# Kernel optimization log

Measured on AMD Instinct MI355X. Metric: run time of the kernel, lower is better.

Reference implementation:

```python
import jax, jax.numpy as jnp
import numpy as np
from jax import lax

MIN_R = 0.01
RADIUS = 0.8
NSAMPLE = 32
PRED_NSAMPLE = 16
TEMPERATURE = 1.0
DIV_COEF = 10.0
GRID3 = 64  # grid_size**3, grid_size=4
EPS = 1e-5


def _ball_query(q, xyz, radius, nsample):
    """q (M,3), xyz (N,3), radius scalar or (M,). Returns idx (M,nsample) int32, empty (M,) bool.
    Mirrors stack ball_query CUDA op: first-found neighbors within radius, padded with first index."""
    N = xyz.shape[0]
    d2 = jnp.sum((q[:, None, :] - xyz[None, :, :]) ** 2, axis=-1)  # (M,N)
    r = jnp.broadcast_to(jnp.asarray(radius, d2.dtype), (q.shape[0],))[:, None]
    valid = d2 < r * r
    score = jnp.where(valid, -jnp.arange(N, dtype=jnp.int32), -(N + 1))
    vals, _ = lax.top_k(score, nsample)  # largest score == smallest valid index
    idx = -vals
    pad = idx == (N + 1)
    idx = jnp.where(pad, idx[:, :1], idx)  # pad with first found neighbor
    empty = pad[:, 0]                       # no neighbor at all
    idx = jnp.where(empty[:, None], 0, idx)
    return idx, empty


def _group(q, xyz, feats, idx, empty):
    """QueryAndGroup gather: relative xyz concat point features; zero empty queries.
    Returns (M, nsample, 3+C)."""
    g_xyz = xyz[idx] - q[:, None, :]
    g = jnp.concatenate([g_xyz, feats[idx]], axis=-1)
    return jnp.where(empty[:, None, None], jnp.zeros((), g.dtype), g)


def _mlp(x, params):
    """Shared 1x1 Conv2d + BatchNorm2d(training stats) + ReLU stack. x: (B,M,S,C)."""
    for W, g, b in params:
        x = jnp.einsum('bmsc,cd->bmsd', x, W)
        mu = x.mean(axis=(0, 1, 2))
        var = x.var(axis=(0, 1, 2))
        x = (x - mu) * lax.rsqrt(var + EPS) * g + b
        x = jax.nn.relu(x)
    return x


def setup_inputs() -> dict:
    key = jax.random.key(0)
    ks = jax.random.split(key, 16)
    B, N, C, R, Croi = 2, 8192, 32, 64, 128
    scene = jnp.array([10.0, 10.0, 4.0], jnp.float32)
    xyz = jax.random.uniform(ks[0], (B, N, 3), jnp.float32) * scene
    features = jax.random.normal(ks[1], (B, N, C), jnp.float32)
    rois = jax.random.uniform(ks[2], (B, R, GRID3, 3), jnp.float32) * scene
    roi_features = jax.random.normal(ks[3], (B, R, Croi), jnp.float32)

    def kaiming(k, fi, fo):
        return jax.random.normal(k, (fi, fo), jnp.float32) * np.float32(np.sqrt(2.0 / fi))

    return {
        'xyz': xyz, 'features': features, 'rois': rois, 'roi_features': roi_features,
        'temperature_decay': jnp.ones((1,), jnp.float32),
        # predict mlp: [32+3, 32, 32]
        'pw0': kaiming(ks[4], 35, 32), 'pg0': jnp.ones(32), 'pb0': jnp.zeros(32),
        'pw1': kaiming(ks[5], 32, 32), 'pg1': jnp.ones(32), 'pb1': jnp.zeros(32),
        # feat mlp: [32+3, 64, 64]
        'fw0': kaiming(ks[6], 35, 64), 'fg0': jnp.ones(64), 'fb0': jnp.zeros(64),
        'fw1': kaiming(ks[7], 64, 64), 'fg1': jnp.ones(64), 'fb1': jnp.zeros(64),
        # predict fc: [32*64 + 128, 1]
        'fcw': kaiming(ks[8], 2176, 1), 'fcb': jnp.zeros(1),
    }


def reference(xyz, features, rois, roi_features, temperature_decay,
              pw0, pg0, pb0, pw1, pg1, pb1,
              fw0, fg0, fb0, fw1, fg1, fb1, fcw, fcb):
    B, num_rois = rois.shape[0], rois.shape[1]
    new_xyz = rois.reshape(B, -1, 3)  # (B, M, 3), M = num_rois*grid^3

    # ---- radius-prediction branch: fixed-radius grouping + MLP + max-pool ----
    idx_p, empty_p = jax.vmap(lambda q, x: _ball_query(q, x, RADIUS, PRED_NSAMPLE))(new_xyz, xyz)
    gp = jax.vmap(_group)(new_xyz, xyz, features, idx_p, empty_p)  # (B,M,S,3+C)
    gp = _mlp(gp, [(pw0, pg0, pb0), (pw1, pg1, pb1)])
    pooled = gp.max(axis=2)                       # (B, M, Cp)
    pooled = pooled.reshape(B, num_rois, -1)      # (B, R, grid^3*Cp)
    res = jnp.concatenate([pooled, roi_features], axis=-1) @ fcw + fcb  # (B,R,1)
    r = jnp.maximum(res / DIV_COEF + RADIUS, MIN_R)
    r_pts = jnp.broadcast_to(r, (B, num_rois, GRID3)).reshape(B, -1)    # (B, M)

    # ---- deformable branch: per-query radius grouping + soft weights ----
    idx_d, empty_d = jax.vmap(lambda q, x, rr: _ball_query(q, x, rr, NSAMPLE))(new_xyz, xyz, r_pts)
    gd = jax.vmap(_group)(new_xyz, xyz, features, idx_d, empty_d)       # (B,M,S,3+C)
    dist = jnp.linalg.norm(gd[..., :3], axis=-1)                        # (B,M,S)
    w = jax.nn.sigmoid((r_pts[..., None] - dist) / (TEMPERATURE * temperature_decay[0]))
    w = jnp.where(empty_d[..., None], jnp.zeros((), w.dtype), w)
    gd = _mlp(gd, [(fw0, fg0, fb0), (fw1, fg1, fb1)])                   # (B,M,S,Cout)
    new_feats = (w[..., None] * gd).max(axis=2)                          # (B,M,Cout)

    return new_xyz.reshape(-1, 3), new_feats.reshape(-1, new_feats.shape[-1])
```

## Files before the change

kernel.cpp:

```cpp
#include <hip/hip_runtime.h>
#include <hip/hip_fp16.h>

#define NB 2
#define NPTS 8192
#define NQ 4096
#define MTOT 8192
#define SP 16
#define SD 32
#define CIN 32
#define CP 32
#define CF 64
#define NROI 128
#define RADIUS_C 0.8f
#define MIN_R_C 0.01f
#define DIV_COEF_C 10.0f

#define INV_CS 1.25f
#define NCX 13
#define NCY 13
#define NCZ 5
#define NCELL (NCX * NCY * NCZ)

__device__ int    g_idx_p[MTOT * SP];
__device__ int    g_empty_p[MTOT];
__device__ int    g_idx_d[MTOT * SD];
__device__ int    g_empty_d[MTOT];
__device__ int    g_cellcnt[NB][NCELL];
__device__ int    g_cellcur[NB][NCELL];
__device__ int    g_cellstart[NB][NCELL + 1];
__device__ float4 g_cellxyzw[NB][NPTS];
__device__ unsigned char g_xa[(size_t)MTOT * SD * CF * 2];
__device__ unsigned char g_xb[(size_t)MTOT * SD * CF * 2];
__device__ unsigned int g_w1h[CF * CF / 2];
__device__ float g_psT[CF * 2048];
__device__ float g_pqT[CF * 2048];
__device__ float g_bnscale[4][CF];
__device__ float g_bnshift[4][CF];
__device__ float g_pdot[MTOT];
__device__ float g_rroi[NROI];

typedef _Float16 h2v __attribute__((ext_vector_type(2)));
__device__ __forceinline__ float fdot2f(unsigned int a, unsigned int b, float c) {
#if defined(__has_builtin)
#if __has_builtin(__builtin_amdgcn_fdot2)
    h2v ha, hb;
    ha = *(h2v*)&a; hb = *(h2v*)&b;
    return __builtin_amdgcn_fdot2(ha, hb, c, false);
#else
    __half2 ha = *(__half2*)&a, hb = *(__half2*)&b;
    float2 fa = __half22float2(ha), fb = __half22float2(hb);
    return fmaf(fa.x, fb.x, fmaf(fa.y, fb.y, c));
#endif
#else
    __half2 ha = *(__half2*)&a, hb = *(__half2*)&b;
    float2 fa = __half22float2(ha), fb = __half22float2(hb);
    return fmaf(fa.x, fb.x, fmaf(fa.y, fb.y, c));
#endif
}

__global__ void copy_xyz_kernel(const float* __restrict__ rois, float* __restrict__ out) {
    int i = blockIdx.x * 256 + threadIdx.x;
    if (i < MTOT * 3) out[i] = rois[i];
}

__global__ void prep_w1_kernel(const float* __restrict__ fw1) {
    int i = blockIdx.x * 256 + threadIdx.x;
    if (i >= CF * CF / 2) return;
    int ch = i >> 5, c2 = i & 31;
    __half2 h = __floats2half2_rn(fw1[(2 * c2) * CF + ch], fw1[(2 * c2 + 1) * CF + ch]);
    g_w1h[i] = *(unsigned int*)&h;
}

__global__ void grid_zero_kernel() {
    int i = blockIdx.x * 1024 + threadIdx.x;
    if (i < NB * NCELL) ((int*)g_cellcnt)[i] = 0;
}

__device__ __forceinline__ int cell_of(float x, float y, float z) {
    int cx = min(NCX - 1, max(0, (int)floorf(x * INV_CS)));
    int cy = min(NCY - 1, max(0, (int)floorf(y * INV_CS)));
    int cz = min(NCZ - 1, max(0, (int)floorf(z * INV_CS)));
    return (cz * NCY + cy) * NCX + cx;
}

__global__ void grid_count_kernel(const float* __restrict__ xyz) {
    int i = blockIdx.x * 256 + threadIdx.x;
    int b = i >> 13;
    int cell = cell_of(xyz[(size_t)i * 3 + 0], xyz[(size_t)i * 3 + 1], xyz[(size_t)i * 3 + 2]);
    atomicAdd(&g_cellcnt[b][cell], 1);
}

__global__ void grid_prefix_kernel() {
    __shared__ int sc[1024];
    int b = blockIdx.x, tid = threadIdx.x;
    int v = (tid < NCELL) ? g_cellcnt[b][tid] : 0;
    sc[tid] = v;
    __syncthreads();
    for (int off = 1; off < 1024; off <<= 1) {
        int add = (tid >= off) ? sc[tid - off] : 0;
        __syncthreads();
        sc[tid] += add;
        __syncthreads();
    }
    if (tid < NCELL) {
        int excl = sc[tid] - v;
        g_cellstart[b][tid] = excl;
        g_cellcur[b][tid] = excl;
    }
    if (tid == 0) g_cellstart[b][NCELL] = NPTS;
}

__global__ void grid_scatter_kernel(const float* __restrict__ xyz) {
    int i = blockIdx.x * 256 + threadIdx.x;
    int b = i >> 13, il = i & (NPTS - 1);
    float x = xyz[(size_t)i * 3 + 0];
    float y = xyz[(size_t)i * 3 + 1];
    float z = xyz[(size_t)i * 3 + 2];
    int cell = cell_of(x, y, z);
    int pos = atomicAdd(&g_cellcur[b][cell], 1);
    g_cellxyzw[b][pos] = make_float4(x, y, z, __int_as_float(il));
}

template <int NS>
__launch_bounds__(256, 8)
__global__ void bq_grid_kernel(const float* __restrict__ xyz, const float* __restrict__ newxyz) {
    __shared__ int s_epos[4][1024];
    int tid = threadIdx.x, wv = tid >> 6, lane = tid & 63;
    int q = blockIdx.x * 4 + wv;
    int b = q >> 12;
    float qx = newxyz[q * 3 + 0], qy = newxyz[q * 3 + 1], qz = newxyz[q * 3 + 2];
    float r = (NS == SP) ? RADIUS_C : g_rroi[q >> 6];
    float r2 = r * r;
    int* idx_out   = (NS == SP) ? g_idx_p   : g_idx_d;
    int* empty_out = (NS == SP) ? g_empty_p : g_empty_d;

    float rp = r + 1e-4f;
    int xlo = max(0, min(NCX - 1, (int)floorf((qx - rp) * INV_CS)));
    int xhi = max(0, min(NCX - 1, (int)floorf((qx + rp) * INV_CS)));
    int ylo = max(0, min(NCY - 1, (int)floorf((qy - rp) * INV_CS)));
    int yhi = max(0, min(NCY - 1, (int)floorf((qy + rp) * INV_CS)));
    int zlo = max(0, min(NCZ - 1, (int)floorf((qz - rp) * INV_CS)));
    int zhi = max(0, min(NCZ - 1, (int)floorf((qz + rp) * INV_CS)));
    int nx = xhi - xlo + 1, ny = yhi - ylo + 1, nz = zhi - zlo + 1;
    int ncell = nx * ny * nz;

    int T = 0;
    bool fb = (ncell > 512);
    if (!fb) {
        for (int c0 = 0; c0 < ncell; c0 += 64) {
            int ci = c0 + lane;
            int cstart = 0, ccnt = 0;
            if (ci < ncell) {
                int cx = xlo + (ci % nx);
                int t1 = ci / nx;
                int cy = ylo + (t1 % ny);
                int cz = zlo + (t1 / ny);
                int cell = (cz * NCY + cy) * NCX + cx;
                cstart = g_cellstart[b][cell];
                ccnt = g_cellstart[b][cell + 1] - cstart;
            }
            int incl = ccnt;
#pragma unroll
            for (int off = 1; off < 64; off <<= 1) {
                int n = __shfl_up(incl, off, 64);
                if (lane >= off) incl += n;
            }
            int chunkT = __shfl(incl, 63, 64);
            int pre = T + incl - ccnt;
            if (T + chunkT <= 1024) {
                for (int k = 0; k < ccnt; ++k) s_epos[wv][pre + k] = cstart + k;
            }
            T += chunkT;
        }
        if (T > 1024) fb = true;
    }

    if (fb) {
        const float* xb = xyz + (size_t)b * NPTS * 3;
        int cnt2 = 0, first_idx = 0;
        for (int g = 0; g < NPTS / 64 && cnt2 < NS; ++g) {
            int p = (g << 6) + lane;
            float dx = qx - xb[3 * p + 0];
            float dy = qy - xb[3 * p + 1];
            float dz = qz - xb[3 * p + 2];
            bool valid = (dx * dx + dy * dy + dz * dz) < r2;
            unsigned long long mask = __ballot(valid);
            if (cnt2 == 0 && mask) first_idx = (g << 6) + (int)__builtin_ctzll(mask);
            int pos = cnt2 + __popcll(mask & ((1ull << lane) - 1ull));
            if (valid && pos < NS) idx_out[q * NS + pos] = p;
            cnt2 += (int)__popcll(mask);
        }
        if (cnt2 == 0) {
            if (lane < NS) idx_out[q * NS + lane] = 0;
            if (lane == 0) empty_out[q] = 1;
        } else {
            int filled = cnt2 < NS ? cnt2 : NS;
            if (lane >= filled && lane < NS) idx_out[q * NS + lane] = first_idx;
            if (lane == 0) empty_out[q] = 0;
        }
        return;
    }
    __asm__ volatile("s_waitcnt lgkmcnt(0)" ::: "memory");

    int p[16];
#pragma unroll
    for (int k = 0; k < 16; ++k) {
        int t = k * 64 + lane;
        int pk = 0x7FFFFFFF;
        if (t < T) {
            int e = s_epos[wv][t];
            float4 v = g_cellxyzw[b][e];
            float dx = qx - v.x, dy = qy - v.y, dz = qz - v.z;
            if (dx * dx + dy * dy + dz * dz < r2) pk = __float_as_int(v.w);
        }
        p[k] = pk;
    }

    int lcnt = 0, lmin = 0x7FFFFFFF;
#pragma unroll
    for (int k = 0; k < 16; ++k) {
        if (p[k] != 0x7FFFFFFF) { ++lcnt; lmin = min(lmin, p[k]); }
    }
    int cnt = lcnt, fidx = lmin;
#pragma unroll
    for (int off = 1; off < 64; off <<= 1) {
        cnt += __shfl_xor(cnt, off, 64);
        fidx = min(fidx, __shfl_xor(fidx, off, 64));
    }
    if (cnt == 0) {
        if (lane < NS) idx_out[q * NS + lane] = 0;
        if (lane == 0) empty_out[q] = 1;
        return;
    }
    int thr = 0x7FFFFFFF;
    if (cnt > NS) {
        int lo = 0, hi = NPTS;
        while (lo < hi) {
            int mid = (lo + hi) >> 1;
            int c = 0;
#pragma unroll
            for (int k = 0; k < 16; ++k) c += (p[k] < mid) ? 1 : 0;
#pragma unroll
            for (int off = 1; off < 64; off <<= 1) c += __shfl_xor(c, off, 64);
            if (c >= NS) hi = mid; else lo = mid + 1;
        }
        thr = lo;
    }
    int qc = 0;
#pragma unroll
    for (int k = 0; k < 16; ++k) qc += (p[k] < thr) ? 1 : 0;
    int qincl = qc;
#pragma unroll
    for (int off = 1; off < 64; off <<= 1) {
        int n = __shfl_up(qincl, off, 64);
        if (lane >= off) qincl += n;
    }
    int pos = qincl - qc;
#pragma unroll
    for (int k = 0; k < 16; ++k) {
        if (p[k] < thr) {
            if (pos < NS) idx_out[q * NS + pos] = p[k];
            ++pos;
        }
    }
    if (lane >= cnt && lane < NS) idx_out[q * NS + lane] = fidx;
    if (lane == 0) empty_out[q] = 0;
}

template <int NS, int CH, bool HALF>
__launch_bounds__(128, 4)
__global__ void mlp_passA_kernel(const float* __restrict__ xyz, const float* __restrict__ feats,
                                 const float* __restrict__ newxyz, const float* __restrict__ W0,
                                 void* __restrict__ xout_) {
    constexpr int GSTR = 37;
    constexpr int SST  = CH + 2;
    __shared__ float buf[128 * GSTR];
    __shared__ float ls[128], lq[128];
    int tid = threadIdx.x;
    int rowbase = blockIdx.x * 128;
    int row = rowbase + tid;
    int q = row / NS, b = q >> 12;
    const int* idx_arr = (NS == SP) ? g_idx_p : g_idx_d;
    const int* emp_arr = (NS == SP) ? g_empty_p : g_empty_d;
    {
        float* dst = &buf[tid * GSTR];
        if (emp_arr[q]) {
#pragma unroll
            for (int c = 0; c < 35; ++c) dst[c] = 0.f;
        } else {
            int idx = idx_arr[row];
            const float* xp = xyz + (size_t)b * NPTS * 3 + idx * 3;
            dst[0] = xp[0] - newxyz[q * 3 + 0];
            dst[1] = xp[1] - newxyz[q * 3 + 1];
            dst[2] = xp[2] - newxyz[q * 3 + 2];
            const float4* fp = (const float4*)(feats + (size_t)b * NPTS * CIN + (size_t)idx * CIN);
#pragma unroll
            for (int j = 0; j < 8; ++j) {
                float4 v = fp[j];
                dst[3 + 4 * j + 0] = v.x; dst[3 + 4 * j + 1] = v.y;
                dst[3 + 4 * j + 2] = v.z; dst[3 + 4 * j + 3] = v.w;
            }
        }
    }
    float acc[CH];
#pragma unroll
    for (int ch = 0; ch < CH; ++ch) acc[ch] = 0.f;
    {
        const float* inrow = &buf[tid * GSTR];
        for (int c = 0; c < 35; ++c) {
            float h = inrow[c];
#pragma unroll
            for (int ch = 0; ch < CH; ++ch) acc[ch] = fmaf(h, W0[c * CH + ch], acc[ch]);
        }
    }
    float* xf = (float*)xout_;
    __half* xh = (__half*)xout_;
    float sum = 0.f, sq = 0.f;
#pragma unroll
    for (int p = 0; p < 2; ++p) {
        __syncthreads();
        if ((tid >> 6) == p) {
            float* srow = &buf[(tid & 63) * SST];
#pragma unroll
            for (int ch = 0; ch < CH; ++ch) srow[ch] = acc[ch];
        }
        __syncthreads();
        if (CH == 64) {
            int ch = tid & 63, rg = tid >> 6;
            for (int r = 0; r < 32; ++r) {
                float v = buf[(rg * 32 + r) * SST + ch];
                size_t o = (size_t)(rowbase + p * 64 + rg * 32 + r) * CH + ch;
                if (HALF) xh[o] = __float2half_rn(v); else xf[o] = v;
                sum += v; sq += v * v;
            }
        } else {
            int ch = tid & 31, rg = tid >> 5;
            for (int r = 0; r < 16; ++r) {
                float v = buf[(rg * 16 + r) * SST + ch];
                size_t o = (size_t)(rowbase + p * 64 + rg * 16 + r) * CH + ch;
                if (HALF) xh[o] = __float2half_rn(v); else xf[o] = v;
                sum += v; sq += v * v;
            }
        }
    }
    ls[tid] = sum; lq[tid] = sq;
    __syncthreads();
    if (CH == 64) {
        if (tid < 64) {
            g_psT[tid * 2048 + blockIdx.x] = ls[tid] + ls[64 + tid];
            g_pqT[tid * 2048 + blockIdx.x] = lq[tid] + lq[64 + tid];
        }
    } else {
        if (tid < 32) {
            g_psT[tid * 2048 + blockIdx.x] = ls[tid] + ls[32 + tid] + ls[64 + tid] + ls[96 + tid];
            g_pqT[tid * 2048 + blockIdx.x] = lq[tid] + lq[32 + tid] + lq[64 + tid] + lq[96 + tid];
        }
    }
}

template <int NS, int CH>
__launch_bounds__(128, 4)
__global__ void mlp_passB_kernel(const float* __restrict__ W1, const float* __restrict__ xin,
                                 float* __restrict__ xout, int bn0) {
    constexpr int HSTR = 33;
    constexpr int SST  = CH + 2;
    __shared__ float buf[128 * 37];
    __shared__ float ls[128], lq[128];
    int tid = threadIdx.x;
    int rowbase = blockIdx.x * 128;
    const float* sc0 = g_bnscale[bn0];
    const float* sh0 = g_bnshift[bn0];
    float acc2[CH];
#pragma unroll
    for (int ch = 0; ch < CH; ++ch) acc2[ch] = 0.f;
    const float4* src = (const float4*)xin;
#pragma unroll
    for (int hc = 0; hc < CH / 32; ++hc) {
        if (hc) __syncthreads();
#pragma unroll
        for (int k = 0; k < 8; ++k) {
            int o4 = tid + k * 128;
            int rloc = o4 >> 3, j = o4 & 7;
            int c = 4 * j, gc = hc * 32 + c;
            float4 v = src[(size_t)(rowbase + rloc) * (CH / 4) + hc * 8 + j];
            float* d = &buf[rloc * HSTR + c];
            d[0] = fmaxf(fmaf(v.x, sc0[gc + 0], sh0[gc + 0]), 0.f);
            d[1] = fmaxf(fmaf(v.y, sc0[gc + 1], sh0[gc + 1]), 0.f);
            d[2] = fmaxf(fmaf(v.z, sc0[gc + 2], sh0[gc + 2]), 0.f);
            d[3] = fmaxf(fmaf(v.w, sc0[gc + 3], sh0[gc + 3]), 0.f);
        }
        __syncthreads();
        const float* hrow = &buf[tid * HSTR];
        for (int c = 0; c < 32; ++c) {
            float h = hrow[c];
#pragma unroll
            for (int ch = 0; ch < CH; ++ch)
                acc2[ch] = fmaf(h, W1[(hc * 32 + c) * CH + ch], acc2[ch]);
        }
    }
    float sum = 0.f, sq = 0.f;
#pragma unroll
    for (int p = 0; p < 2; ++p) {
        __syncthreads();
        if ((tid >> 6) == p) {
            float* srow = &buf[(tid & 63) * SST];
#pragma unroll
            for (int ch = 0; ch < CH; ++ch) srow[ch] = acc2[ch];
        }
        __syncthreads();
        int ch = tid & 31, rg = tid >> 5;
        for (int r = 0; r < 16; ++r) {
            float v = buf[(rg * 16 + r) * SST + ch];
            xout[(size_t)(rowbase + p * 64 + rg * 16 + r) * CH + ch] = v;
            sum += v; sq += v * v;
        }
    }
    ls[tid] = sum; lq[tid] = sq;
    __syncthreads();
    if (tid < 32) {
        g_psT[tid * 2048 + blockIdx.x] = ls[tid] + ls[32 + tid] + ls[64 + tid] + ls[96 + tid];
        g_pqT[tid * 2048 + blockIdx.x] = lq[tid] + lq[32 + tid] + lq[64 + tid] + lq[96 + tid];
    }
}

__launch_bounds__(128, 4)
__global__ void mlp_fB_kernel(const __half* __restrict__ xin, __half* __restrict__ xout) {
    __shared__ unsigned int hp[128 * 37];
    __shared__ float ls[128], lq[128];
    int tid = threadIdx.x;
    int rowbase = blockIdx.x * 128;
    const float* sc0 = g_bnscale[2];
    const float* sh0 = g_bnshift[2];
    {
        const float4* src = (const float4*)xin;
#pragma unroll
        for (int k = 0; k < 8; ++k) {
            int o4 = tid + k * 128;
            int rloc = o4 >> 3, j = o4 & 7;
            float4 v = src[(size_t)(rowbase + rloc) * 8 + j];
            const __half2* ph = (const __half2*)&v;
            unsigned int* d = &hp[rloc * 37 + 4 * j];
#pragma unroll
            for (int m = 0; m < 4; ++m) {
                float2 f = __half22float2(ph[m]);
                int gc = 8 * j + 2 * m;
                float a = fmaxf(fmaf(f.x, sc0[gc + 0], sh0[gc + 0]), 0.f);
                float bb = fmaxf(fmaf(f.y, sc0[gc + 1], sh0[gc + 1]), 0.f);
                __half2 hh = __floats2half2_rn(a, bb);
                d[m] = *(unsigned int*)&hh;
            }
        }
    }
    __syncthreads();
    float acc2[CF];
#pragma unroll
    for (int ch = 0; ch < CF; ++ch) acc2[ch] = 0.f;
    {
        const unsigned int* hrow = &hp[tid * 37];
#pragma unroll
        for (int c2 = 0; c2 < 32; ++c2) {
            unsigned int h2 = hrow[c2];
#pragma unroll
            for (int ch = 0; ch < CF; ++ch)
                acc2[ch] = fdot2f(h2, g_w1h[ch * 32 + c2], acc2[ch]);
        }
    }
    {
        unsigned int orow[32];
#pragma unroll
        for (int m = 0; m < 32; ++m) {
            __half2 hh = __floats2half2_rn(acc2[2 * m], acc2[2 * m + 1]);
            orow[m] = *(unsigned int*)&hh;
        }
        uint4* dst = (uint4*)(xout + (size_t)(rowbase + tid) * CF);
#pragma unroll
        for (int m = 0; m < 8; ++m)
            dst[m] = make_uint4(orow[4 * m], orow[4 * m + 1], orow[4 * m + 2], orow[4 * m + 3]);
    }
    float* fview = (float*)hp;
    float sum = 0.f, sq = 0.f;
#pragma unroll
    for (int p = 0; p < 2; ++p) {
        __syncthreads();
        if ((tid >> 6) == p) {
            float* srow = &fview[(tid & 63) * 66];
#pragma unroll
            for (int ch = 0; ch < CF; ++ch) srow[ch] = acc2[ch];
        }
        __syncthreads();
        int ch = tid & 63, rg = tid >> 6;
        for (int r = 0; r < 32; ++r) {
            float v = fview[(rg * 32 + r) * 66 + ch];
            sum += v; sq += v * v;
        }
    }
    ls[tid] = sum; lq[tid] = sq;
    __syncthreads();
    if (tid < 64) {
        g_psT[tid * 2048 + blockIdx.x] = ls[tid] + ls[64 + tid];
        g_pqT[tid * 2048 + blockIdx.x] = lq[tid] + lq[64 + tid];
    }
}

__global__ void passC_f_kernel(const float* __restrict__ xyz, const float* __restrict__ newxyz,
                               const float* __restrict__ td, const __half* __restrict__ xin,
                               float* __restrict__ out) {
    __shared__ float lw[64];
    int tid = threadIdx.x;
    int qpair = blockIdx.x * 2;
    if (tid < 64) {
        int ql = tid >> 5, s = tid & 31;
        int q = qpair + ql;
        float wv = 0.f;
        if (!g_empty_d[q]) {
            int idx = g_idx_d[q * SD + s];
            int b = q >> 12;
            float dx = xyz[(size_t)b * NPTS * 3 + idx * 3 + 0] - newxyz[q * 3 + 0];
            float dy = xyz[(size_t)b * NPTS * 3 + idx * 3 + 1] - newxyz[q * 3 + 1];
            float dz = xyz[(size_t)b * NPTS * 3 + idx * 3 + 2] - newxyz[q * 3 + 2];
            float dist = sqrtf(dx * dx + dy * dy + dz * dz);
            float rq = g_rroi[q >> 6];
            wv = 1.f / (1.f + expf(-(rq - dist) / td[0]));
        }
        lw[tid] = wv;
    }
    __syncthreads();
    int ql = tid >> 6, ch = tid & 63;
    int q = qpair + ql;
    float sc = g_bnscale[3][ch], sh = g_bnshift[3][ch];
    float m = 0.f;
    for (int s = 0; s < SD; ++s) {
        float v = __half2float(xin[((size_t)q * SD + s) * CF + ch]);
        m = fmaxf(m, lw[ql * 32 + s] * fmaxf(fmaf(v, sc, sh), 0.f));
    }
    out[MTOT * 3 + (size_t)q * CF + ch] = m;
}

__global__ void passC_p_kernel(const float* __restrict__ fcw, const float* __restrict__ xin) {
    int tid = threadIdx.x;
    int q = blockIdx.x * 8 + (tid >> 5);
    int ch = tid & 31;
    float sc = g_bnscale[1][ch], sh = g_bnshift[1][ch];
    float m = 0.f;
    for (int s = 0; s < SP; ++s) {
        float v = xin[(size_t)(q * SP + s) * CP + ch] * sc + sh;
        m = fmaxf(m, fmaxf(v, 0.f));
    }
    float pd = m * fcw[(q & 63) * CP + ch];
    for (int off = 16; off > 0; off >>= 1) pd += __shfl_down(pd, off, 32);
    if (ch == 0) g_pdot[q] = pd;
}

__global__ void finalize_kernel(const float* __restrict__ gamma, const float* __restrict__ beta,
                                float n, int layer, int nblocks) {
    __shared__ double l_s[256], l_q[256];
    int ch = blockIdx.x, tid = threadIdx.x;
    double s = 0, q = 0;
    for (int i = tid; i < nblocks; i += 256) { s += g_psT[ch * 2048 + i]; q += g_pqT[ch * 2048 + i]; }
    l_s[tid] = s; l_q[tid] = q; __syncthreads();
    for (int off = 128; off > 0; off >>= 1) {
        if (tid < off) { l_s[tid] += l_s[tid + off]; l_q[tid] += l_q[tid + off]; }
        __syncthreads();
    }
    if (tid == 0) {
        double mu = l_s[0] / (double)n;
        double var = l_q[0] / (double)n - mu * mu;
        if (var < 0) var = 0;
        double sc = (double)gamma[ch] / sqrt(var + 1e-5);
        g_bnscale[layer][ch] = (float)sc;
        g_bnshift[layer][ch] = (float)((double)beta[ch] - mu * sc);
    }
}

__global__ void roi_r_kernel(const float* __restrict__ roif, const float* __restrict__ fcw,
                             const float* __restrict__ fcb) {
    int tid = threadIdx.x;
    int roi = blockIdx.x * 4 + (tid >> 6);
    int lane = tid & 63;
    float acc = g_pdot[roi * 64 + lane]
              + roif[roi * 128 + lane]      * fcw[2048 + lane]
              + roif[roi * 128 + 64 + lane] * fcw[2048 + 64 + lane];
    for (int off = 32; off > 0; off >>= 1) acc += __shfl_down(acc, off, 64);
    if (lane == 0) {
        float res = acc + fcb[0];
        g_rroi[roi] = fmaxf(res / DIV_COEF_C + RADIUS_C, MIN_R_C);
    }
}

extern "C" void kernel_launch(void* const* d_in, const int* in_sizes, int n_in,
                              void* d_out, int out_size, void* d_ws, size_t ws_size,
                              hipStream_t stream) {
    const float* xyz   = (const float*)d_in[0];
    const float* feats = (const float*)d_in[1];
    const float* rois  = (const float*)d_in[2];
    const float* roif  = (const float*)d_in[3];
    const float* td    = (const float*)d_in[4];
    const float* pw0 = (const float*)d_in[5];
    const float* pg0 = (const float*)d_in[6];
    const float* pb0 = (const float*)d_in[7];
    const float* pw1 = (const float*)d_in[8];
    const float* pg1 = (const float*)d_in[9];
    const float* pb1 = (const float*)d_in[10];
    const float* fw0 = (const float*)d_in[11];
    const float* fg0 = (const float*)d_in[12];
    const float* fb0 = (const float*)d_in[13];
    const float* fw1 = (const float*)d_in[14];
    const float* fg1 = (const float*)d_in[15];
    const float* fb1 = (const float*)d_in[16];
    const float* fcw = (const float*)d_in[17];
    const float* fcb = (const float*)d_in[18];
    float* out = (float*)d_out;

    void* xa; hipGetSymbolAddress(&xa, HIP_SYMBOL(g_xa));
    void* xb; hipGetSymbolAddress(&xb, HIP_SYMBOL(g_xb));

    copy_xyz_kernel<<<96, 256, 0, stream>>>(rois, out);
    prep_w1_kernel<<<8, 256, 0, stream>>>(fw1);

    grid_zero_kernel<<<2, 1024, 0, stream>>>();
    grid_count_kernel<<<64, 256, 0, stream>>>(xyz);
    grid_prefix_kernel<<<2, 1024, 0, stream>>>();
    grid_scatter_kernel<<<64, 256, 0, stream>>>(xyz);

    bq_grid_kernel<SP><<<MTOT / 4, 256, 0, stream>>>(xyz, rois);
    mlp_passA_kernel<SP, CP, false><<<1024, 128, 0, stream>>>(xyz, feats, rois, pw0, xa);
    finalize_kernel<<<CP, 256, 0, stream>>>(pg0, pb0, (float)(MTOT * SP), 0, 1024);
    mlp_passB_kernel<SP, CP><<<1024, 128, 0, stream>>>(pw1, (const float*)xa, (float*)xb, 0);
    finalize_kernel<<<CP, 256, 0, stream>>>(pg1, pb1, (float)(MTOT * SP), 1, 1024);
    passC_p_kernel<<<MTOT / 8, 256, 0, stream>>>(fcw, (const float*)xb);
    roi_r_kernel<<<NROI / 4, 256, 0, stream>>>(roif, fcw, fcb);

    bq_grid_kernel<SD><<<MTOT / 4, 256, 0, stream>>>(xyz, rois);
    mlp_passA_kernel<SD, CF, true><<<2048, 128, 0, stream>>>(xyz, feats, rois, fw0, xa);
    finalize_kernel<<<CF, 256, 0, stream>>>(fg0, fb0, (float)(MTOT * SD), 2, 2048);
    mlp_fB_kernel<<<2048, 128, 0, stream>>>((const __half*)xa, (__half*)xb);
    finalize_kernel<<<CF, 256, 0, stream>>>(fg1, fb1, (float)(MTOT * SD), 3, 2048);
    passC_f_kernel<<<MTOT / 2, 128, 0, stream>>>(xyz, rois, td, (const __half*)xb, out);
}
```

Before: 267.9 us.

## Fuse BN finalize into MLP kernels, merge setup kernels, rewrite ball-query selection

Replaces the separate finalize kernels with a last-block-done tail that accumulates batch-norm statistics through double atomics, removing four launches. The setup kernels and the ROI radius kernels are each merged into one. The ball query is rewritten to test candidates directly per cell, append hits to shared memory with atomics, and pick the first-NS indices by rank counting. mlp_fB now writes its half-precision output from the transposed shared view. The costs are atomic contention, serial per-lane loops over cells, and quadratic rank counting when a query has many hits.

```diff
diff --git a/kernel.cpp b/kernel.cpp
--- a/kernel.cpp
+++ b/kernel.cpp
@@ -32,12 +32,12 @@
 __device__ unsigned char g_xa[(size_t)MTOT * SD * CF * 2];
 __device__ unsigned char g_xb[(size_t)MTOT * SD * CF * 2];
 __device__ unsigned int g_w1h[CF * CF / 2];
-__device__ float g_psT[CF * 2048];
-__device__ float g_pqT[CF * 2048];
-__device__ float g_bnscale[4][CF];
-__device__ float g_bnshift[4][CF];
-__device__ float g_pdot[MTOT];
-__device__ float g_rroi[NROI];
+__device__ double g_bnsum[4][CF];
+__device__ double g_bnsq[4][CF];
+__device__ int    g_bncnt[4];
+__device__ float  g_bnscale[4][CF];
+__device__ float  g_bnshift[4][CF];
+__device__ float  g_rroi[NROI];
 
 typedef _Float16 h2v __attribute__((ext_vector_type(2)));
 __device__ __forceinline__ float fdot2f(unsigned int a, unsigned int b, float c) {
@@ -58,22 +58,31 @@
 #endif
 }
 
-__global__ void copy_xyz_kernel(const float* __restrict__ rois, float* __restrict__ out) {
-    int i = blockIdx.x * 256 + threadIdx.x;
-    if (i < MTOT * 3) out[i] = rois[i];
-}
-
-__global__ void prep_w1_kernel(const float* __restrict__ fw1) {
-    int i = blockIdx.x * 256 + threadIdx.x;
-    if (i >= CF * CF / 2) return;
-    int ch = i >> 5, c2 = i & 31;
-    __half2 h = __floats2half2_rn(fw1[(2 * c2) * CF + ch], fw1[(2 * c2 + 1) * CF + ch]);
-    g_w1h[i] = *(unsigned int*)&h;
-}
-
-__global__ void grid_zero_kernel() {
-    int i = blockIdx.x * 1024 + threadIdx.x;
-    if (i < NB * NCELL) ((int*)g_cellcnt)[i] = 0;
+__device__ __forceinline__ void bn_tail(int layer, float ps, float pq, int chans,
+                                        int tid, int nblocks, float n,
+                                        const float* gamma, const float* beta,
+                                        int* lastflag) {
+    if (tid < chans) {
+        atomicAdd(&g_bnsum[layer][tid], (double)ps);
+        atomicAdd(&g_bnsq[layer][tid], (double)pq);
+    }
+    __syncthreads();
+    if (tid == 0) {
+        __threadfence();
+        int old = atomicAdd(&g_bncnt[layer], 1);
+        *lastflag = (old == nblocks - 1);
+    }
+    __syncthreads();
+    if (*lastflag && tid < chans) {
+        double s = atomicAdd(&g_bnsum[layer][tid], 0.0);
+        double qq = atomicAdd(&g_bnsq[layer][tid], 0.0);
+        double mu = s / (double)n;
+        double var = qq / (double)n - mu * mu;
+        if (var < 0) var = 0;
+        double sc = (double)gamma[tid] / sqrt(var + 1e-5);
+        g_bnscale[layer][tid] = (float)sc;
+        g_bnshift[layer][tid] = (float)((double)beta[tid] - mu * sc);
+    }
 }
 
 __device__ __forceinline__ int cell_of(float x, float y, float z) {
@@ -81,6 +90,28 @@
     int cy = min(NCY - 1, max(0, (int)floorf(y * INV_CS)));
     int cz = min(NCZ - 1, max(0, (int)floorf(z * INV_CS)));
     return (cz * NCY + cy) * NCX + cx;
+}
+
+#define SETUP_N (MTOT * 3 + CF * CF / 2 + NB * NCELL + 4 * CF * 2 + 4)
+__global__ void setup_kernel(const float* __restrict__ rois, const float* __restrict__ fw1,
+                             float* __restrict__ out) {
+    int i = blockIdx.x * 256 + threadIdx.x;
+    if (i < MTOT * 3) { out[i] = rois[i]; return; }
+    i -= MTOT * 3;
+    if (i < CF * CF / 2) {
+        int ch = i >> 5, c2 = i & 31;
+        __half2 h = __floats2half2_rn(fw1[(2 * c2) * CF + ch], fw1[(2 * c2 + 1) * CF + ch]);
+        g_w1h[i] = *(unsigned int*)&h;
+        return;
+    }
+    i -= CF * CF / 2;
+    if (i < NB * NCELL) { ((int*)g_cellcnt)[i] = 0; return; }
+    i -= NB * NCELL;
+    if (i < 4 * CF) { ((double*)g_bnsum)[i] = 0.0; return; }
+    i -= 4 * CF;
+    if (i < 4 * CF) { ((double*)g_bnsq)[i] = 0.0; return; }
+    i -= 4 * CF;
+    if (i < 4) g_bncnt[i] = 0;
 }
 
 __global__ void grid_count_kernel(const float* __restrict__ xyz) {
@@ -124,7 +155,8 @@
 template <int NS>
 __launch_bounds__(256, 8)
 __global__ void bq_grid_kernel(const float* __restrict__ xyz, const float* __restrict__ newxyz) {
-    __shared__ int s_epos[4][1024];
+    __shared__ int s_cand[4][512];
+    __shared__ int s_meta[4][2];
     int tid = threadIdx.x, wv = tid >> 6, lane = tid & 63;
     int q = blockIdx.x * 4 + wv;
     int b = q >> 12;
@@ -133,6 +165,9 @@
     float r2 = r * r;
     int* idx_out   = (NS == SP) ? g_idx_p   : g_idx_d;
     int* empty_out = (NS == SP) ? g_empty_p : g_empty_d;
+
+    if (lane == 0) s_meta[wv][0] = 0;
+    __asm__ volatile("s_waitcnt lgkmcnt(0)" ::: "memory");
 
     float rp = r + 1e-4f;
     int xlo = max(0, min(NCX - 1, (int)floorf((qx - rp) * INV_CS)));
@@ -144,38 +179,28 @@
     int nx = xhi - xlo + 1, ny = yhi - ylo + 1, nz = zhi - zlo + 1;
     int ncell = nx * ny * nz;
 
-    int T = 0;
-    bool fb = (ncell > 512);
-    if (!fb) {
-        for (int c0 = 0; c0 < ncell; c0 += 64) {
-            int ci = c0 + lane;
-            int cstart = 0, ccnt = 0;
-            if (ci < ncell) {
-                int cx = xlo + (ci % nx);
-                int t1 = ci / nx;
-                int cy = ylo + (t1 % ny);
-                int cz = zlo + (t1 / ny);
-                int cell = (cz * NCY + cy) * NCX + cx;
-                cstart = g_cellstart[b][cell];
-                ccnt = g_cellstart[b][cell + 1] - cstart;
+    bool ovf = false;
+    for (int ci = lane; ci < ncell; ci += 64) {
+        int cx = xlo + (ci % nx);
+        int t1 = ci / nx;
+        int cy = ylo + (t1 % ny);
+        int cz = zlo + (t1 / ny);
+        int cell = (cz * NCY + cy) * NCX + cx;
+        int s0 = g_cellstart[b][cell], e0 = g_cellstart[b][cell + 1];
+        for (int e = s0; e < e0; ++e) {
+            float4 v = g_cellxyzw[b][e];
+            float dx = qx - v.x, dy = qy - v.y, dz = qz - v.z;
+            if (dx * dx + dy * dy + dz * dz < r2) {
+                int pos = atomicAdd(&s_meta[wv][0], 1);
+                if (pos < 512) s_cand[wv][pos] = __float_as_int(v.w);
+                else ovf = true;
             }
-            int incl = ccnt;
-#pragma unroll
-            for (int off = 1; off < 64; off <<= 1) {
-                int n = __shfl_up(incl, off, 64);
-                if (lane >= off) incl += n;
-            }
-            int chunkT = __shfl(incl, 63, 64);
-            int pre = T + incl - ccnt;
-            if (T + chunkT <= 1024) {
-                for (int k = 0; k < ccnt; ++k) s_epos[wv][pre + k] = cstart + k;
-            }
-            T += chunkT;
-        }
-        if (T > 1024) fb = true;
-    }
-
-    if (fb) {
+        }
+    }
+    __asm__ volatile("s_waitcnt lgkmcnt(0) vmcnt(0)" ::: "memory");
+    int cnt = s_meta[wv][0];
+
+    if (__ballot(ovf)) {
         const float* xb = xyz + (size_t)b * NPTS * 3;
         int cnt2 = 0, first_idx = 0;
         for (int g = 0; g < NPTS / 64 && cnt2 < NS; ++g) {
@@ -200,70 +225,21 @@
         }
         return;
     }
-    __asm__ volatile("s_waitcnt lgkmcnt(0)" ::: "memory");
-
-    int p[16];
-#pragma unroll
-    for (int k = 0; k < 16; ++k) {
-        int t = k * 64 + lane;
-        int pk = 0x7FFFFFFF;
-        if (t < T) {
-            int e = s_epos[wv][t];
-            float4 v = g_cellxyzw[b][e];
-            float dx = qx - v.x, dy = qy - v.y, dz = qz - v.z;
-            if (dx * dx + dy * dy + dz * dz < r2) pk = __float_as_int(v.w);
-        }
-        p[k] = pk;
-    }
-
-    int lcnt = 0, lmin = 0x7FFFFFFF;
-#pragma unroll
-    for (int k = 0; k < 16; ++k) {
-        if (p[k] != 0x7FFFFFFF) { ++lcnt; lmin = min(lmin, p[k]); }
-    }
-    int cnt = lcnt, fidx = lmin;
-#pragma unroll
-    for (int off = 1; off < 64; off <<= 1) {
-        cnt += __shfl_xor(cnt, off, 64);
-        fidx = min(fidx, __shfl_xor(fidx, off, 64));
-    }
+
     if (cnt == 0) {
         if (lane < NS) idx_out[q * NS + lane] = 0;
         if (lane == 0) empty_out[q] = 1;
         return;
     }
-    int thr = 0x7FFFFFFF;
-    if (cnt > NS) {
-        int lo = 0, hi = NPTS;
-        while (lo < hi) {
-            int mid = (lo + hi) >> 1;
-            int c = 0;
-#pragma unroll
-            for (int k = 0; k < 16; ++k) c += (p[k] < mid) ? 1 : 0;
-#pragma unroll
-            for (int off = 1; off < 64; off <<= 1) c += __shfl_xor(c, off, 64);
-            if (c >= NS) hi = mid; else lo = mid + 1;
-        }
-        thr = lo;
-    }
-    int qc = 0;
-#pragma unroll
-    for (int k = 0; k < 16; ++k) qc += (p[k] < thr) ? 1 : 0;
-    int qincl = qc;
-#pragma unroll
-    for (int off = 1; off < 64; off <<= 1) {
-        int n = __shfl_up(qincl, off, 64);
-        if (lane >= off) qincl += n;
-    }
-    int pos = qincl - qc;
-#pragma unroll
-    for (int k = 0; k < 16; ++k) {
-        if (p[k] < thr) {
-            if (pos < NS) idx_out[q * NS + pos] = p[k];
-            ++pos;
-        }
-    }
-    if (lane >= cnt && lane < NS) idx_out[q * NS + lane] = fidx;
+    for (int i = lane; i < cnt; i += 64) {
+        int c = s_cand[wv][i];
+        int rank = 0;
+        for (int j = 0; j < cnt; ++j) rank += (s_cand[wv][j] < c) ? 1 : 0;
+        if (rank < NS) idx_out[q * NS + rank] = c;
+        if (rank == 0) s_meta[wv][1] = c;
+    }
+    __asm__ volatile("s_waitcnt lgkmcnt(0)" ::: "memory");
+    if (cnt < NS && lane >= cnt && lane < NS) idx_out[q * NS + lane] = s_meta[wv][1];
     if (lane == 0) empty_out[q] = 0;
 }
 
@@ -271,11 +247,14 @@
 __launch_bounds__(128, 4)
 __global__ void mlp_passA_kernel(const float* __restrict__ xyz, const float* __restrict__ feats,
                                  const float* __restrict__ newxyz, const float* __restrict__ W0,
-                                 void* __restrict__ xout_) {
+                                 void* __restrict__ xout_,
+                                 const float* __restrict__ gamma, const float* __restrict__ beta,
+                                 int layer, float n) {
     constexpr int GSTR = 37;
     constexpr int SST  = CH + 2;
     __shared__ float buf[128 * GSTR];
     __shared__ float ls[128], lq[128];
+    __shared__ int lastf;
     int tid = threadIdx.x;
     int rowbase = blockIdx.x * 128;
     int row = rowbase + tid;
@@ -345,27 +324,29 @@
     }
     ls[tid] = sum; lq[tid] = sq;
     __syncthreads();
+    float ps = 0.f, pq = 0.f;
     if (CH == 64) {
-        if (tid < 64) {
-            g_psT[tid * 2048 + blockIdx.x] = ls[tid] + ls[64 + tid];
-            g_pqT[tid * 2048 + blockIdx.x] = lq[tid] + lq[64 + tid];
-        }
+        if (tid < 64) { ps = ls[tid] + ls[64 + tid]; pq = lq[tid] + lq[64 + tid]; }
     } else {
         if (tid < 32) {
-            g_psT[tid * 2048 + blockIdx.x] = ls[tid] + ls[32 + tid] + ls[64 + tid] + ls[96 + tid];
-            g_pqT[tid * 2048 + blockIdx.x] = lq[tid] + lq[32 + tid] + lq[64 + tid] + lq[96 + tid];
-        }
-    }
+            ps = ls[tid] + ls[32 + tid] + ls[64 + tid] + ls[96 + tid];
+            pq = lq[tid] + lq[32 + tid] + lq[64 + tid] + lq[96 + tid];
+        }
+    }
+    bn_tail(layer, ps, pq, CH, tid, gridDim.x, n, gamma, beta, &lastf);
 }
 
 template <int NS, int CH>
 __launch_bounds__(128, 4)
 __global__ void mlp_passB_kernel(const float* __restrict__ W1, const float* __restrict__ xin,
-                                 float* __restrict__ xout, int bn0) {
+                                 float* __restrict__ xout, int bn0,
+                                 const float* __restrict__ gamma, const float* __restrict__ beta,
+                                 int layer, float n) {
     constexpr int HSTR = 33;
     constexpr int SST  = CH + 2;
     __shared__ float buf[128 * 37];
     __shared__ float ls[128], lq[128];
+    __shared__ int lastf;
     int tid = threadIdx.x;
     int rowbase = blockIdx.x * 128;
     const float* sc0 = g_bnscale[bn0];
@@ -417,16 +398,20 @@
     }
     ls[tid] = sum; lq[tid] = sq;
     __syncthreads();
+    float ps = 0.f, pq = 0.f;
     if (tid < 32) {
-        g_psT[tid * 2048 + blockIdx.x] = ls[tid] + ls[32 + tid] + ls[64 + tid] + ls[96 + tid];
-        g_pqT[tid * 2048 + blockIdx.x] = lq[tid] + lq[32 + tid] + lq[64 + tid] + lq[96 + tid];
-    }
+        ps = ls[tid] + ls[32 + tid] + ls[64 + tid] + ls[96 + tid];
+        pq = lq[tid] + lq[32 + tid] + lq[64 + tid] + lq[96 + tid];
+    }
+    bn_tail(layer, ps, pq, CH, tid, gridDim.x, n, gamma, beta, &lastf);
 }
 
 __launch_bounds__(128, 4)
-__global__ void mlp_fB_kernel(const __half* __restrict__ xin, __half* __restrict__ xout) {
+__global__ void mlp_fB_kernel(const __half* __restrict__ xin, __half* __restrict__ xout,
+                              const float* __restrict__ gamma, const float* __restrict__ beta) {
     __shared__ unsigned int hp[128 * 37];
     __shared__ float ls[128], lq[128];
+    __shared__ int lastf;
     int tid = threadIdx.x;
     int rowbase = blockIdx.x * 128;
     const float* sc0 = g_bnscale[2];
@@ -465,18 +450,6 @@
                 acc2[ch] = fdot2f(h2, g_w1h[ch * 32 + c2], acc2[ch]);
         }
     }
-    {
-        unsigned int orow[32];
-#pragma unroll
-        for (int m = 0; m < 32; ++m) {
-            __half2 hh = __floats2half2_rn(acc2[2 * m], acc2[2 * m + 1]);
-            orow[m] = *(unsigned int*)&hh;
-        }
-        uint4* dst = (uint4*)(xout + (size_t)(rowbase + tid) * CF);
-#pragma unroll
-        for (int m = 0; m < 8; ++m)
-            dst[m] = make_uint4(orow[4 * m], orow[4 * m + 1], orow[4 * m + 2], orow[4 * m + 3]);
-    }
     float* fview = (float*)hp;
     float sum = 0.f, sq = 0.f;
 #pragma unroll
@@ -491,15 +464,15 @@
         int ch = tid & 63, rg = tid >> 6;
         for (int r = 0; r < 32; ++r) {
             float v = fview[(rg * 32 + r) * 66 + ch];
+            xout[(size_t)(rowbase + p * 64 + rg * 32 + r) * CF + ch] = __float2half_rn(v);
             sum += v; sq += v * v;
         }
     }
     ls[tid] = sum; lq[tid] = sq;
     __syncthreads();
-    if (tid < 64) {
-        g_psT[tid * 2048 + blockIdx.x] = ls[tid] + ls[64 + tid];
-        g_pqT[tid * 2048 + blockIdx.x] = lq[tid] + lq[64 + tid];
-    }
+    float ps = 0.f, pq = 0.f;
+    if (tid < 64) { ps = ls[tid] + ls[64 + tid]; pq = lq[tid] + lq[64 + tid]; }
+    bn_tail(3, ps, pq, CF, tid, gridDim.x, (float)(MTOT * SD), gamma, beta, &lastf);
 }
 
 __global__ void passC_f_kernel(const float* __restrict__ xyz, const float* __restrict__ newxyz,
@@ -536,55 +509,32 @@
     out[MTOT * 3 + (size_t)q * CF + ch] = m;
 }
 
-__global__ void passC_p_kernel(const float* __restrict__ fcw, const float* __restrict__ xin) {
+__global__ void passC_roi_kernel(const float* __restrict__ fcw, const float* __restrict__ fcb,
+                                 const float* __restrict__ roif, const float* __restrict__ xin) {
+    __shared__ float red[256];
     int tid = threadIdx.x;
-    int q = blockIdx.x * 8 + (tid >> 5);
-    int ch = tid & 31;
+    int roi = blockIdx.x;
+    int ch = tid & 31, qs = tid >> 5;
     float sc = g_bnscale[1][ch], sh = g_bnshift[1][ch];
-    float m = 0.f;
-    for (int s = 0; s < SP; ++s) {
-        float v = xin[(size_t)(q * SP + s) * CP + ch] * sc + sh;
-        m = fmaxf(m, fmaxf(v, 0.f));
-    }
-    float pd = m * fcw[(q & 63) * CP + ch];
-    for (int off = 16; off > 0; off >>= 1) pd += __shfl_down(pd, off, 32);
-    if (ch == 0) g_pdot[q] = pd;
-}
-
-__global__ void finalize_kernel(const float* __restrict__ gamma, const float* __restrict__ beta,
-                                float n, int layer, int nblocks) {
-    __shared__ double l_s[256], l_q[256];
-    int ch = blockIdx.x, tid = threadIdx.x;
-    double s = 0, q = 0;
-    for (int i = tid; i < nblocks; i += 256) { s += g_psT[ch * 2048 + i]; q += g_pqT[ch * 2048 + i]; }
-    l_s[tid] = s; l_q[tid] = q; __syncthreads();
+    float acc = 0.f;
+    for (int ql = qs; ql < 64; ql += 8) {
+        int q = roi * 64 + ql;
+        float m = 0.f;
+        for (int s = 0; s < SP; ++s) {
+            float v = xin[(size_t)(q * SP + s) * CP + ch] * sc + sh;
+            m = fmaxf(m, fmaxf(v, 0.f));
+        }
+        acc += m * fcw[ql * CP + ch];
+    }
+    if (tid < 128) acc += roif[roi * 128 + tid] * fcw[2048 + tid];
+    red[tid] = acc;
+    __syncthreads();
     for (int off = 128; off > 0; off >>= 1) {
-        if (tid < off) { l_s[tid] += l_s[tid + off]; l_q[tid] += l_q[tid + off]; }
-        __syncthreads();
-    }
-    if (tid == 0) {
-        double mu = l_s[0] / (double)n;
-        double var = l_q[0] / (double)n - mu * mu;
-        if (var < 0) var = 0;
-        double sc = (double)gamma[ch] / sqrt(var + 1e-5);
-        g_bnscale[layer][ch] = (float)sc;
-        g_bnshift[layer][ch] = (float)((double)beta[ch] - mu * sc);
-    }
-}
-
-__global__ void roi_r_kernel(const float* __restrict__ roif, const float* __restrict__ fcw,
-                             const float* __restrict__ fcb) {
-    int tid = threadIdx.x;
-    int roi = blockIdx.x * 4 + (tid >> 6);
-    int lane = tid & 63;
-    float acc = g_pdot[roi * 64 + lane]
-              + roif[roi * 128 + lane]      * fcw[2048 + lane]
-              + roif[roi * 128 + 64 + lane] * fcw[2048 + 64 + lane];
-    for (int off = 32; off > 0; off >>= 1) acc += __shfl_down(acc, off, 64);
-    if (lane == 0) {
-        float res = acc + fcb[0];
-        g_rroi[roi] = fmaxf(res / DIV_COEF_C + RADIUS_C, MIN_R_C);
-    }
+        if (tid < off) red[tid] += red[tid + off];
+        __syncthreads();
+    }
+    if (tid == 0)
+        g_rroi[roi] = fmaxf((red[0] + fcb[0]) / DIV_COEF_C + RADIUS_C, MIN_R_C);
 }
 
 extern "C" void kernel_launch(void* const* d_in, const int* in_sizes, int n_in,
@@ -614,26 +564,21 @@
     void* xa; hipGetSymbolAddress(&xa, HIP_SYMBOL(g_xa));
     void* xb; hipGetSymbolAddress(&xb, HIP_SYMBOL(g_xb));
 
-    copy_xyz_kernel<<<96, 256, 0, stream>>>(rois, out);
-    prep_w1_kernel<<<8, 256, 0, stream>>>(fw1);
-
-    grid_zero_kernel<<<2, 1024, 0, stream>>>();
+    setup_kernel<<<(SETUP_N + 255) / 256, 256, 0, stream>>>(rois, fw1, out);
     grid_count_kernel<<<64, 256, 0, stream>>>(xyz);
     grid_prefix_kernel<<<2, 1024, 0, stream>>>();
     grid_scatter_kernel<<<64, 256, 0, stream>>>(xyz);
 
     bq_grid_kernel<SP><<<MTOT / 4, 256, 0, stream>>>(xyz, rois);
-    mlp_passA_kernel<SP, CP, false><<<1024, 128, 0, stream>>>(xyz, feats, rois, pw0, xa);
-    finalize_kernel<<<CP, 256, 0, stream>>>(pg0, pb0, (float)(MTOT * SP), 0, 1024);
-    mlp_passB_kernel<SP, CP><<<1024, 128, 0, stream>>>(pw1, (const float*)xa, (float*)xb, 0);
-    finalize_kernel<<<CP, 256, 0, stream>>>(pg1, pb1, (float)(MTOT * SP), 1, 1024);
-    passC_p_kernel<<<MTOT / 8, 256, 0, stream>>>(fcw, (const float*)xb);
-    roi_r_kernel<<<NROI / 4, 256, 0, stream>>>(roif, fcw, fcb);
+    mlp_passA_kernel<SP, CP, false><<<1024, 128, 0, stream>>>(xyz, feats, rois, pw0, xa,
+                                                              pg0, pb0, 0, (float)(MTOT * SP));
+    mlp_passB_kernel<SP, CP><<<1024, 128, 0, stream>>>(pw1, (const float*)xa, (float*)xb, 0,
+                                                       pg1, pb1, 1, (float)(MTOT * SP));
+    passC_roi_kernel<<<NROI, 256, 0, stream>>>(fcw, fcb, roif, (const float*)xb);
 
     bq_grid_kernel<SD><<<MTOT / 4, 256, 0, stream>>>(xyz, rois);
-    mlp_passA_kernel<SD, CF, true><<<2048, 128, 0, stream>>>(xyz, feats, rois, fw0, xa);
-    finalize_kernel<<<CF, 256, 0, stream>>>(fg0, fb0, (float)(MTOT * SD), 2, 2048);
-    mlp_fB_kernel<<<2048, 128, 0, stream>>>((const __half*)xa, (__half*)xb);
-    finalize_kernel<<<CF, 256, 0, stream>>>(fg1, fb1, (float)(MTOT * SD), 3, 2048);
+    mlp_passA_kernel<SD, CF, true><<<2048, 128, 0, stream>>>(xyz, feats, rois, fw0, xa,
+                                                             fg0, fb0, 2, (float)(MTOT * SD));
+    mlp_fB_kernel<<<2048, 128, 0, stream>>>((const __half*)xa, (__half*)xb, fg1, fb1);
     passC_f_kernel<<<MTOT / 2, 128, 0, stream>>>(xyz, rois, td, (const __half*)xb, out);
 }
```

Result: slower. 436.9 us (+63.1%).
